# Optimization experiments

Hardware: AMD Instinct MI355X
Metric: run time of the kernel (lower is better)

## Reference

```python
import jax, jax.numpy as jnp
import numpy as np

N_NODES = 50000
N_EDGES = 800000
D_FEAT = 64
IN_DIM = 1 + 2 * D_FEAT  # 129
FC_DIMS = [128, 64, 1]


def setup_inputs() -> dict:
    key = jax.random.key(0)
    ks = jax.random.split(key, 10)
    x = jax.random.normal(ks[0], (N_NODES, D_FEAT), dtype=jnp.float32)
    edge_index = jax.random.randint(ks[1], (2, N_EDGES), 0, N_NODES, dtype=jnp.int64)
    edge_weight = jax.random.uniform(ks[2], (N_EDGES, 1), dtype=jnp.float32)
    # MLP params (Linear: y = x @ W.T + b), Kaiming-ish scale
    dims = [IN_DIM] + FC_DIMS
    W1 = jax.random.normal(ks[3], (dims[1], dims[0]), dtype=jnp.float32) / np.sqrt(dims[0])
    b1 = jnp.zeros((dims[1],), dtype=jnp.float32)
    W2 = jax.random.normal(ks[4], (dims[2], dims[1]), dtype=jnp.float32) / np.sqrt(dims[1])
    b2 = jnp.zeros((dims[2],), dtype=jnp.float32)
    W3 = jax.random.normal(ks[5], (dims[3], dims[2]), dtype=jnp.float32) / np.sqrt(dims[2])
    b3 = jnp.zeros((dims[3],), dtype=jnp.float32)
    return {"x": x, "edge_index": edge_index, "edge_weight": edge_weight,
            "W1": W1, "b1": b1, "W2": W2, "b2": b2, "W3": W3, "b3": b3}


def reference(x, edge_index, edge_weight, W1, b1, W2, b2, W3, b3):
    # Gather source/target node features per edge: [E, d]
    src = x[edge_index[0]]
    tgt = x[edge_index[1]]
    # Concat [edge_weight | src | tgt] -> [E, 1 + 2d]
    h = jnp.concatenate([edge_weight, src, tgt], axis=1)
    # MLP (dropout is None / eval; last layer dim==1 -> no ReLU)
    h = jax.nn.relu(h @ W1.T + b1)
    h = jax.nn.relu(h @ W2.T + b2)
    return h @ W3.T + b3  # [E, 1] new edge weights
```

## Files before the change

kernel.cpp:

```cpp
#include <hip/hip_runtime.h>

typedef _Float16 half8 __attribute__((ext_vector_type(8)));
typedef _Float16 half4_t __attribute__((ext_vector_type(4)));
typedef float floatx4 __attribute__((ext_vector_type(4)));

#define LP 136

__global__ __launch_bounds__(256) void prep_kernel(
    const float* __restrict__ x,
    const float* __restrict__ W1, const float* __restrict__ W2,
    _Float16* __restrict__ wsh, _Float16* __restrict__ xh, int n_x8)
{
    int b = blockIdx.x;
    if (b < 96) {
        int tid = b * 256 + threadIdx.x;
        if (tid < 16384) {
            int c = tid >> 9, r = tid & 511;
            int L = r >> 3, jj = r & 7;
            int mt = c >> 2, kb = c & 3;
            int n = mt * 16 + (L & 15);
            int k = kb * 32 + (L >> 4) * 8 + jj;
            wsh[tid] = (_Float16)W1[n * 129 + 1 + k];
        } else {
            int t = tid - 16384;
            int c = t >> 9, r = t & 511;
            int L = r >> 3, jj = r & 7;
            int mt = c >> 2, kb = c & 3;
            int i = mt * 16 + (L & 15);
            int j = kb * 32 + (L >> 4) * 8 + jj;
            wsh[tid] = (_Float16)W2[i * 128 + j];
        }
    } else {
        int t2 = (b - 96) * 256 + threadIdx.x;
        if (t2 < n_x8) {
            const float4* p = (const float4*)(x + (size_t)t2 * 8);
            float4 v0 = p[0], v1 = p[1];
            half8 h = {(_Float16)v0.x, (_Float16)v0.y, (_Float16)v0.z, (_Float16)v0.w,
                       (_Float16)v1.x, (_Float16)v1.y, (_Float16)v1.z, (_Float16)v1.w};
            *(half8*)(xh + (size_t)t2 * 8) = h;
        }
    }
}

__global__ __launch_bounds__(256, 4) void edge_mlp_kernel(
    const _Float16* __restrict__ xh,
    const int* __restrict__ ei,
    const float* __restrict__ ew,
    const float* __restrict__ W1, const float* __restrict__ b1,
    const float* __restrict__ b2,
    const float* __restrict__ W3, const float* __restrict__ b3,
    const _Float16* __restrict__ wf,
    float* __restrict__ out, int E)
{
    __shared__ __align__(16) _Float16 hA[128 * LP];
    __shared__ float s_ew[128];
    __shared__ float s_b1[128];
    __shared__ float s_c0[128];
    __shared__ float s_b2[64];
    __shared__ float s_w3[64];
    __shared__ float s_out[4][128];

    const int tid = threadIdx.x;
    const int e_blk = blockIdx.x * 128;

    if (tid < 128) {
        s_b1[tid] = b1[tid];
        s_c0[tid] = W1[tid * 129];
        int e = e_blk + tid; if (e >= E) e = E - 1;
        s_ew[tid] = ew[e];
    } else if (tid < 192) {
        int i = tid - 128;
        s_b2[i] = b2[i];
        s_w3[i] = W3[i];
    }

    {
        int e_loc = tid >> 1;
        int part = tid & 1;
        int e = e_blk + e_loc; if (e >= E) e = E - 1;
        int node = ei[(size_t)part * E + e];
        const _Float16* rp = xh + (size_t)node * 64;
        _Float16* dst = &hA[e_loc * LP + part * 64];
#pragma unroll
        for (int q = 0; q < 8; ++q)
            *(half8*)(dst + q * 8) = *(const half8*)(rp + q * 8);
    }
    __syncthreads();

    const int lane = tid & 63;
    const int wave = tid >> 6;
    const int lrow = lane & 15;
    const int quad = lane >> 4;

    half8 afr[2][4];
#pragma unroll
    for (int mi = 0; mi < 2; ++mi)
#pragma unroll
        for (int kb = 0; kb < 4; ++kb)
            afr[mi][kb] = *(const half8*)(wf + ((2 * wave + mi) * 4 + kb) * 512 + lane * 8);

    half4_t h1v[2][8];
#pragma unroll
    for (int nt = 0; nt < 8; ++nt) {
        half8 bfr[4];
#pragma unroll
        for (int kb = 0; kb < 4; ++kb)
            bfr[kb] = *(const half8*)(&hA[(nt * 16 + lrow) * LP + kb * 32 + quad * 8]);
        float ewv = s_ew[nt * 16 + lrow];
#pragma unroll
        for (int mi = 0; mi < 2; ++mi) {
            floatx4 a = {0.f, 0.f, 0.f, 0.f};
#pragma unroll
            for (int kb = 0; kb < 4; ++kb)
                a = __builtin_amdgcn_mfma_f32_16x16x32_f16(afr[mi][kb], bfr[kb], a, 0, 0, 0);
            int nb = (2 * wave + mi) * 16 + quad * 4;
            half4_t hv;
#pragma unroll
            for (int r = 0; r < 4; ++r) {
                float v = a[r] + s_b1[nb + r] + ewv * s_c0[nb + r];
                hv[r] = (_Float16)fmaxf(v, 0.f);
            }
            h1v[mi][nt] = hv;
        }
    }
    __syncthreads();

#pragma unroll
    for (int mi = 0; mi < 2; ++mi) {
        int nb = (2 * wave + mi) * 16 + quad * 4;
#pragma unroll
        for (int nt = 0; nt < 8; ++nt)
            *(half4_t*)(&hA[(nt * 16 + lrow) * LP + nb]) = h1v[mi][nt];
    }
    __syncthreads();

    half8 a2fr[4];
#pragma unroll
    for (int kb = 0; kb < 4; ++kb)
        a2fr[kb] = *(const half8*)(wf + 16384 + (wave * 4 + kb) * 512 + lane * 8);

#pragma unroll
    for (int nt = 0; nt < 8; ++nt) {
        half8 bfr[4];
#pragma unroll
        for (int kb = 0; kb < 4; ++kb)
            bfr[kb] = *(const half8*)(&hA[(nt * 16 + lrow) * LP + kb * 32 + quad * 8]);
        floatx4 a = {0.f, 0.f, 0.f, 0.f};
#pragma unroll
        for (int kb = 0; kb < 4; ++kb)
            a = __builtin_amdgcn_mfma_f32_16x16x32_f16(a2fr[kb], bfr[kb], a, 0, 0, 0);
        int ib = wave * 16 + quad * 4;
        float p = 0.f;
#pragma unroll
        for (int r = 0; r < 4; ++r)
            p += fmaxf(a[r] + s_b2[ib + r], 0.f) * s_w3[ib + r];
        p += __shfl_xor(p, 16, 64);
        p += __shfl_xor(p, 32, 64);
        if (quad == 0) s_out[wave][nt * 16 + lrow] = p;
    }
    __syncthreads();

    if (tid < 128) {
        int oe = e_blk + tid;
        if (oe < E)
            out[oe] = b3[0] + s_out[0][tid] + s_out[1][tid]
                            + s_out[2][tid] + s_out[3][tid];
    }
}

extern "C" void kernel_launch(void* const* d_in, const int* in_sizes, int n_in,
                              void* d_out, int out_size, void* d_ws, size_t ws_size,
                              hipStream_t stream) {
    const float* x  = (const float*)d_in[0];
    const int*   ei = (const int*)d_in[1];
    const float* ew = (const float*)d_in[2];
    const float* W1 = (const float*)d_in[3];
    const float* b1 = (const float*)d_in[4];
    const float* W2 = (const float*)d_in[5];
    const float* b2 = (const float*)d_in[6];
    const float* W3 = (const float*)d_in[7];
    const float* b3 = (const float*)d_in[8];
    float* out = (float*)d_out;
    const int E = in_sizes[2];
    const int n_x = in_sizes[0];
    const int n_x8 = n_x / 8;

    _Float16* wsh = (_Float16*)d_ws;
    _Float16* xh  = (_Float16*)((char*)d_ws + 49152);

    int xblk = (n_x8 + 255) / 256;
    prep_kernel<<<96 + xblk, 256, 0, stream>>>(x, W1, W2, wsh, xh, n_x8);

    int nblk = (E + 127) / 128;
    edge_mlp_kernel<<<nblk, 256, 0, stream>>>(xh, ei, ew, W1, b1, b2, W3, b3,
                                              wsh, out, E);
}
```

Baseline: 141.4 us.

## Partition edges per wave so each wave owns its rows and drops block barriers

```diff
diff --git a/kernel.cpp b/kernel.cpp
--- a/kernel.cpp
+++ b/kernel.cpp
@@ -53,21 +53,21 @@
     float* __restrict__ out, int E)
 {
     __shared__ __align__(16) _Float16 hA[128 * LP];
-    __shared__ float s_ew[128];
     __shared__ float s_b1[128];
     __shared__ float s_c0[128];
     __shared__ float s_b2[64];
     __shared__ float s_w3[64];
-    __shared__ float s_out[4][128];
 
     const int tid = threadIdx.x;
     const int e_blk = blockIdx.x * 128;
+    const int lane = tid & 63;
+    const int wave = tid >> 6;
+    const int lrow = lane & 15;
+    const int quad = lane >> 4;
 
     if (tid < 128) {
         s_b1[tid] = b1[tid];
         s_c0[tid] = W1[tid * 129];
-        int e = e_blk + tid; if (e >= E) e = E - 1;
-        s_ew[tid] = ew[e];
     } else if (tid < 192) {
         int i = tid - 128;
         s_b2[i] = b2[i];
@@ -75,8 +75,8 @@
     }
 
     {
-        int e_loc = tid >> 1;
-        int part = tid & 1;
+        int e_loc = wave * 32 + (lane >> 1);
+        int part = lane & 1;
         int e = e_blk + e_loc; if (e >= E) e = E - 1;
         int node = ei[(size_t)part * E + e];
         const _Float16* rp = xh + (size_t)node * 64;
@@ -87,84 +87,79 @@
     }
     __syncthreads();
 
-    const int lane = tid & 63;
-    const int wave = tid >> 6;
-    const int lrow = lane & 15;
-    const int quad = lane >> 4;
+    float ewv[2];
+#pragma unroll
+    for (int et = 0; et < 2; ++et) {
+        int e = e_blk + wave * 32 + et * 16 + lrow;
+        if (e >= E) e = E - 1;
+        ewv[et] = ew[e];
+    }
 
-    half8 afr[2][4];
+    half8 bfr[2][4];
 #pragma unroll
-    for (int mi = 0; mi < 2; ++mi)
+    for (int et = 0; et < 2; ++et)
 #pragma unroll
         for (int kb = 0; kb < 4; ++kb)
-            afr[mi][kb] = *(const half8*)(wf + ((2 * wave + mi) * 4 + kb) * 512 + lane * 8);
+            bfr[et][kb] = *(const half8*)(&hA[(wave * 32 + et * 16 + lrow) * LP + kb * 32 + quad * 8]);
 
-    half4_t h1v[2][8];
 #pragma unroll
-    for (int nt = 0; nt < 8; ++nt) {
-        half8 bfr[4];
+    for (int mt = 0; mt < 8; ++mt) {
+        half8 afr[4];
 #pragma unroll
         for (int kb = 0; kb < 4; ++kb)
-            bfr[kb] = *(const half8*)(&hA[(nt * 16 + lrow) * LP + kb * 32 + quad * 8]);
-        float ewv = s_ew[nt * 16 + lrow];
+            afr[kb] = *(const half8*)(wf + (mt * 4 + kb) * 512 + lane * 8);
+        floatx4 bb = *(const floatx4*)(&s_b1[mt * 16 + quad * 4]);
+        floatx4 cc = *(const floatx4*)(&s_c0[mt * 16 + quad * 4]);
 #pragma unroll
-        for (int mi = 0; mi < 2; ++mi) {
+        for (int et = 0; et < 2; ++et) {
             floatx4 a = {0.f, 0.f, 0.f, 0.f};
 #pragma unroll
             for (int kb = 0; kb < 4; ++kb)
-                a = __builtin_amdgcn_mfma_f32_16x16x32_f16(afr[mi][kb], bfr[kb], a, 0, 0, 0);
-            int nb = (2 * wave + mi) * 16 + quad * 4;
+                a = __builtin_amdgcn_mfma_f32_16x16x32_f16(afr[kb], bfr[et][kb], a, 0, 0, 0);
             half4_t hv;
 #pragma unroll
-            for (int r = 0; r < 4; ++r) {
-                float v = a[r] + s_b1[nb + r] + ewv * s_c0[nb + r];
-                hv[r] = (_Float16)fmaxf(v, 0.f);
-            }
-            h1v[mi][nt] = hv;
+            for (int r = 0; r < 4; ++r)
+                hv[r] = (_Float16)fmaxf(a[r] + bb[r] + ewv[et] * cc[r], 0.f);
+            *(half4_t*)(&hA[(wave * 32 + et * 16 + lrow) * LP + mt * 16 + quad * 4]) = hv;
         }
     }
-    __syncthreads();
 
+    half8 b2fr[2][4];
 #pragma unroll
-    for (int mi = 0; mi < 2; ++mi) {
-        int nb = (2 * wave + mi) * 16 + quad * 4;
-#pragma unroll
-        for (int nt = 0; nt < 8; ++nt)
-            *(half4_t*)(&hA[(nt * 16 + lrow) * LP + nb]) = h1v[mi][nt];
-    }
-    __syncthreads();
-
-    half8 a2fr[4];
-#pragma unroll
-    for (int kb = 0; kb < 4; ++kb)
-        a2fr[kb] = *(const half8*)(wf + 16384 + (wave * 4 + kb) * 512 + lane * 8);
-
-#pragma unroll
-    for (int nt = 0; nt < 8; ++nt) {
-        half8 bfr[4];
+    for (int et = 0; et < 2; ++et)
 #pragma unroll
         for (int kb = 0; kb < 4; ++kb)
-            bfr[kb] = *(const half8*)(&hA[(nt * 16 + lrow) * LP + kb * 32 + quad * 8]);
-        floatx4 a = {0.f, 0.f, 0.f, 0.f};
+            b2fr[et][kb] = *(const half8*)(&hA[(wave * 32 + et * 16 + lrow) * LP + kb * 32 + quad * 8]);
+
+    float p[2] = {0.f, 0.f};
+#pragma unroll
+    for (int mt = 0; mt < 4; ++mt) {
+        half8 afr[4];
 #pragma unroll
         for (int kb = 0; kb < 4; ++kb)
-            a = __builtin_amdgcn_mfma_f32_16x16x32_f16(a2fr[kb], bfr[kb], a, 0, 0, 0);
-        int ib = wave * 16 + quad * 4;
-        float p = 0.f;
+            afr[kb] = *(const half8*)(wf + 16384 + (mt * 4 + kb) * 512 + lane * 8);
+        floatx4 bb = *(const floatx4*)(&s_b2[mt * 16 + quad * 4]);
+        floatx4 ww = *(const floatx4*)(&s_w3[mt * 16 + quad * 4]);
 #pragma unroll
-        for (int r = 0; r < 4; ++r)
-            p += fmaxf(a[r] + s_b2[ib + r], 0.f) * s_w3[ib + r];
-        p += __shfl_xor(p, 16, 64);
-        p += __shfl_xor(p, 32, 64);
-        if (quad == 0) s_out[wave][nt * 16 + lrow] = p;
+        for (int et = 0; et < 2; ++et) {
+            floatx4 a = {0.f, 0.f, 0.f, 0.f};
+#pragma unroll
+            for (int kb = 0; kb < 4; ++kb)
+                a = __builtin_amdgcn_mfma_f32_16x16x32_f16(afr[kb], b2fr[et][kb], a, 0, 0, 0);
+#pragma unroll
+            for (int r = 0; r < 4; ++r)
+                p[et] += fmaxf(a[r] + bb[r], 0.f) * ww[r];
+        }
     }
-    __syncthreads();
-
-    if (tid < 128) {
-        int oe = e_blk + tid;
-        if (oe < E)
-            out[oe] = b3[0] + s_out[0][tid] + s_out[1][tid]
-                            + s_out[2][tid] + s_out[3][tid];
+#pragma unroll
+    for (int et = 0; et < 2; ++et) {
+        p[et] += __shfl_xor(p[et], 16, 64);
+        p[et] += __shfl_xor(p[et], 32, 64);
+    }
+    float b3v = b3[0];
+    if (quad < 2) {
+        int oe = e_blk + wave * 32 + quad * 16 + lrow;
+        if (oe < E) out[oe] = b3v + p[quad];
     }
 }
 
```

Measured after the change: 150.1 us. +6.2%, slower.
